# Performance work log

Measured on AMD Instinct MI355X. Metric: run time of the kernel, lower is better.

## Reference

```python
import jax, jax.numpy as jnp
import numpy as np
from jax import lax

B, CIN, H, W = 32, 256, 64, 64
K, STRIDE = 9, 2
CAPS_TYPES, OS0, OS1 = 32, 8, 1
NUM_ITER = 3
OH = (H - K) // STRIDE + 1  # 28
OW = (W - K) // STRIDE + 1  # 28
EPS = 1e-8


def squash(x):
    # Hinton squash over capsule pose dims (os0, os1)
    n2 = jnp.sum(x * x, axis=(-2, -1), keepdims=True)
    return (n2 / (1.0 + n2)) * x / jnp.sqrt(n2 + EPS)


def setup_inputs() -> dict:
    key = jax.random.key(0)
    k1, k2 = jax.random.split(key)
    x = jax.random.normal(k1, (B, CIN, H, W), jnp.float32)
    cout = CAPS_TYPES * OS0 * OS1
    conv_w = jax.random.normal(k2, (cout, CIN, K, K), jnp.float32) / np.float32(np.sqrt(CIN * K * K))
    conv_b = jnp.zeros((cout,), jnp.float32)
    routing_bias = jnp.full((CAPS_TYPES, OH, OW, OS0, OS1), 0.1, jnp.float32)
    return {"x": x, "conv_w": conv_w, "conv_b": conv_b, "routing_bias": routing_bias}


def reference(x, conv_w, conv_b, routing_bias):
    b = x.shape[0]
    caps = lax.conv_general_dilated(
        x, conv_w, (STRIDE, STRIDE), 'VALID',
        dimension_numbers=('NCHW', 'OIHW', 'NCHW'))
    caps = caps + conv_b[None, :, None, None]
    # [b, C*os0*os1, oh, ow] -> [b, C, oh, ow, os0, os1]
    caps = caps.reshape(b, CAPS_TYPES, OS0, OS1, OH, OW).transpose(0, 1, 4, 5, 2, 3)
    poses = squash(caps)
    # Dynamic routing (degenerate: one vote per output capsule, singleton input dims)
    votes = poses  # [b, C, oh, ow, os0, os1]
    logits = jnp.zeros((b, CAPS_TYPES, OH, OW), caps.dtype)
    for _ in range(NUM_ITER):
        c = jax.nn.softmax(logits, axis=1)           # couplings over output caps types
        s = c[..., None, None] * votes + routing_bias  # weighted vote sum (+ bias)
        poses = squash(s)
        logits = logits + jnp.sum(votes * poses, axis=(-2, -1))  # agreement update
    acts = jnp.sqrt(jnp.sum(poses * poses, axis=(-2, -1)))  # [b, C, oh, ow]
    return poses, acts
```

## Files before the change

### kernel.cpp

```cpp
#include <hip/hip_runtime.h>

#define B_    32
#define CIN_  256
#define H_    64
#define W_    64
#define OH_   28
#define OW_   28
#define M_TOTAL 25088
#define POSE_ELEMS 6422528

typedef _Float16 f16;
typedef _Float16 f16x8 __attribute__((ext_vector_type(8)));
typedef _Float16 f16x4 __attribute__((ext_vector_type(4)));
typedef float    f32x4 __attribute__((ext_vector_type(4)));

#define GLD_LDS16(gp, lp) __builtin_amdgcn_global_load_lds( \
    (const __attribute__((address_space(1))) void*)(gp),    \
    (__attribute__((address_space(3))) void*)(lp), 16, 0, 0)

#define SBAR()    asm volatile("s_barrier" ::: "memory")
#define WAITVM0() asm volatile("s_waitcnt vmcnt(0)" ::: "memory")
#define WAITVM4() asm volatile("s_waitcnt vmcnt(4)" ::: "memory")
#define LGKM8()   asm volatile("s_waitcnt lgkmcnt(8)" ::: "memory")

__global__ __launch_bounds__(256) void xt_kernel(const float* __restrict__ x,
                                                 f16* __restrict__ Xt)
{
    __shared__ float tile[64 * 65];
    const int t  = threadIdx.x;
    const int c0 = blockIdx.x * 64;
    const int h  = blockIdx.y;
    const int b  = blockIdx.z;

    const float* src = x + (((long)(b * CIN_ + c0)) * H_ + h) * W_;
    const int w4 = (t & 15) * 4;
    const int cr = t >> 4;
#pragma unroll
    for (int it = 0; it < 4; ++it) {
        const int c = it * 16 + cr;
        const float4 v = *(const float4*)(src + (long)c * (H_ * W_) + w4);
        tile[c * 65 + w4 + 0] = v.x;
        tile[c * 65 + w4 + 1] = v.y;
        tile[c * 65 + w4 + 2] = v.z;
        tile[c * 65 + w4 + 3] = v.w;
    }
    __syncthreads();

    f16* dst = Xt + ((long)(b * H_ + h) * W_) * CIN_ + c0;
    const int wq = t >> 4, cq = t & 15;
#pragma unroll
    for (int it = 0; it < 4; ++it) {
        const int w2 = it * 16 + wq;
        f16x4 v;
        v[0] = (f16)tile[(cq * 4 + 0) * 65 + w2];
        v[1] = (f16)tile[(cq * 4 + 1) * 65 + w2];
        v[2] = (f16)tile[(cq * 4 + 2) * 65 + w2];
        v[3] = (f16)tile[(cq * 4 + 3) * 65 + w2];
        *(f16x4*)(dst + (long)w2 * CIN_ + cq * 4) = v;
    }
}

__global__ __launch_bounds__(256) void wt_kernel(const float* __restrict__ w,
                                                 f16* __restrict__ Wt)
{
    __shared__ float tile[64 * 81];
    const int t  = threadIdx.x;
    const int co = blockIdx.x >> 2;
    const int c0 = (blockIdx.x & 3) * 64;
    const float* src = w + ((long)co * 256 + c0) * 81;
    for (int i = t; i < 64 * 81; i += 256) tile[i] = src[i];
    __syncthreads();
    for (int i = t; i < 64 * 81; i += 256) {
        const int khw = i >> 6, ci = i & 63;
        Wt[(long)khw * 65536 + co * 256 + c0 + ci] = (f16)tile[ci * 81 + khw];
    }
}

__global__ __launch_bounds__(512, 2) void gemm_kernel(const f16* __restrict__ Xt,
                                                      const f16* __restrict__ Wt,
                                                      f16* __restrict__ part,
                                                      int nsplit)
{
    __shared__ __align__(16) char lds[131072];
    char* ldsA = lds;
    char* ldsB = lds + 65536;

    const int t    = threadIdx.x;
    const int lane = t & 63, wave = t >> 6;

    const int nwg = 98 * nsplit;
    const int q = nwg >> 3, r8 = nwg & 7;
    const int xcd = blockIdx.x & 7, idx = blockIdx.x >> 3;
    const int wgid = (xcd < r8 ? xcd * (q + 1) : r8 * (q + 1) + (xcd - r8) * q) + idx;
    const int sk = wgid / 98;
    const int mt = wgid - sk * 98;
    const int m0 = mt * 256;

    const int ntb = 324 / nsplit, rem = 324 - ntb * nsplit;
    const int ksb = sk * ntb + (sk < rem ? sk : rem);
    const int NT  = ntb + (sk < rem ? 1 : 0);

    const int csrc = ((lane & 7) ^ (lane >> 3)) * 8;
    int aoff[4], boff[4];
#pragma unroll
    for (int i = 0; i < 4; ++i) {
        const int r  = (i * 8 + wave) * 8 + (lane >> 3);
        const int ga = (r & 63) + ((r >> 6) & 1) * 128 + (r >> 7) * 64;
        const int m  = m0 + ga;
        const int b   = m / 784;
        const int rem2 = m - b * 784;
        const int oh  = rem2 / 28;
        const int ow  = rem2 - oh * 28;
        aoff[i] = ((b * 64 + 2 * oh) * 64 + 2 * ow) * 256 + csrc;
        const int gb = (r & 31) + ((r >> 5) & 3) * 64 + (r >> 7) * 32;
        boff[i] = gb * 256 + csrc;
    }

    const int wm = wave >> 2, wn = wave & 3;
    int rowA[8], rowB[4];
#pragma unroll
    for (int mf = 0; mf < 8; ++mf) {
        const int g  = wm * 128 + mf * 16 + (lane & 15);
        const int lr = (g & 63) + ((g >> 6) & 1) * 128 + (g >> 7) * 64;
        rowA[mf] = lr * 128;
    }
#pragma unroll
    for (int nf = 0; nf < 4; ++nf) {
        const int g  = wn * 64 + nf * 16 + (lane & 15);
        const int lr = (g & 31) + ((g >> 6) << 5) + ((g >> 5) & 1) * 128;
        rowB[nf] = lr * 128;
    }
    int csw[2];
    csw[0] = ((lane >> 4) * 16) ^ ((lane & 7) << 4);
    csw[1] = 64 ^ csw[0];

    f32x4 acc[8][4];
    const f32x4 z = {0.f, 0.f, 0.f, 0.f};
#pragma unroll
    for (int i = 0; i < 8; ++i)
#pragma unroll
        for (int j = 0; j < 4; ++j) acc[i][j] = z;

#define KOFFS(KS, AK, BK)                                      \
    {  const int cb_ = (KS) & 3, khw_ = (KS) >> 2;             \
       const int kh_ = khw_ / 9, kw_ = khw_ - kh_ * 9;         \
       AK = (kh_ * 64 + kw_) * 256 + cb_ * 64;                 \
       BK = khw_ * 65536 + cb_ * 64; }

#define STAGE_A_HALF(H, AK, NB) do {                                               \
    GLD_LDS16(Xt + aoff[2*(H)]   + (AK), ldsA + (NB)*32768 + ((2*(H))*8   + wave)*1024); \
    GLD_LDS16(Xt + aoff[2*(H)+1] + (AK), ldsA + (NB)*32768 + ((2*(H)+1)*8 + wave)*1024); } while(0)
#define STAGE_B_HALF(H, BK, NB) do {                                               \
    GLD_LDS16(Wt + boff[2*(H)]   + (BK), ldsB + (NB)*32768 + ((2*(H))*8   + wave)*1024); \
    GLD_LDS16(Wt + boff[2*(H)+1] + (BK), ldsB + (NB)*32768 + ((2*(H)+1)*8 + wave)*1024); } while(0)

#define MFMA_PAIR(MI, NI, A, Bf)                                                        \
    acc[MI][NI] = __builtin_amdgcn_mfma_f32_16x16x32_f16((A)[0], (Bf)[0], acc[MI][NI], 0,0,0); \
    acc[MI][NI] = __builtin_amdgcn_mfma_f32_16x16x32_f16((A)[1], (Bf)[1], acc[MI][NI], 0,0,0);
#define MFMA_Q(MH, NH, BF)                                          \
    MFMA_PAIR((MH)*4+0, (NH)*2+0, af[0], BF[0]) MFMA_PAIR((MH)*4+0, (NH)*2+1, af[0], BF[1]) \
    MFMA_PAIR((MH)*4+1, (NH)*2+0, af[1], BF[0]) MFMA_PAIR((MH)*4+1, (NH)*2+1, af[1], BF[1]) \
    MFMA_PAIR((MH)*4+2, (NH)*2+0, af[2], BF[0]) MFMA_PAIR((MH)*4+2, (NH)*2+1, af[2], BF[1]) \
    MFMA_PAIR((MH)*4+3, (NH)*2+0, af[3], BF[0]) MFMA_PAIR((MH)*4+3, (NH)*2+1, af[3], BF[1])

#define READ_AF(P, MH) do {                                           \
    _Pragma("unroll")                                                 \
    for (int k_ = 0; k_ < 4; ++k_) {                                  \
        af[k_][0] = *(const f16x8*)((P) + rowA[(MH)*4+k_] + csw[0]);  \
        af[k_][1] = *(const f16x8*)((P) + rowA[(MH)*4+k_] + csw[1]);  \
    } } while(0)
#define READ_BF(P, V, NH) do {                                        \
    _Pragma("unroll")                                                 \
    for (int k_ = 0; k_ < 2; ++k_) {                                  \
        V[k_][0] = *(const f16x8*)((P) + rowB[(NH)*2+k_] + csw[0]);   \
        V[k_][1] = *(const f16x8*)((P) + rowB[(NH)*2+k_] + csw[1]);   \
    } } while(0)

    f16x8 af[4][2], bf0[2][2], bf1[2][2];

    {
        int ak0, bk0;
        KOFFS(ksb, ak0, bk0);
        STAGE_A_HALF(0, ak0, 0);
        STAGE_B_HALF(0, bk0, 0);
        STAGE_B_HALF(1, bk0, 0);
        STAGE_A_HALF(1, ak0, 0);
    }
    WAITVM4();
    SBAR();

#pragma unroll 1
    for (int tt = 0; tt < NT; ++tt) {
        const int c = tt & 1, nc = c ^ 1;
        const int ksn = ksb + ((tt + 1 < NT) ? tt + 1 : tt);
        int akn, bkn;
        KOFFS(ksn, akn, bkn);
        const char* pA = ldsA + c * 32768;
        const char* pB = ldsB + c * 32768;

        STAGE_A_HALF(0, akn, nc);
        WAITVM4();
        READ_AF(pA, 0);
        READ_BF(pB, bf0, 0);
        LGKM8();
        SBAR();
        __builtin_amdgcn_s_setprio(1);
        MFMA_Q(0, 0, bf0)
        __builtin_amdgcn_s_setprio(0);

        STAGE_B_HALF(0, bkn, nc);
        WAITVM4();
        READ_BF(pB, bf1, 1);
        SBAR();
        __builtin_amdgcn_s_setprio(1);
        MFMA_Q(0, 1, bf1)
        __builtin_amdgcn_s_setprio(0);

        STAGE_B_HALF(1, bkn, nc);
        READ_AF(pA, 1);
        SBAR();
        __builtin_amdgcn_s_setprio(1);
        MFMA_Q(1, 1, bf1)
        __builtin_amdgcn_s_setprio(0);

        STAGE_A_HALF(1, akn, nc);
        WAITVM4();
        SBAR();
        __builtin_amdgcn_s_setprio(1);
        MFMA_Q(1, 0, bf0)
        __builtin_amdgcn_s_setprio(0);
    }
    WAITVM0();

    f16* base = part + (long)sk * (M_TOTAL * 256);
    const int lrow = (lane >> 4) * 4;
#pragma unroll
    for (int nf = 0; nf < 4; ++nf) {
        const int n = wn * 64 + nf * 16 + (lane & 15);
#pragma unroll
        for (int mf = 0; mf < 8; ++mf) {
            const long mrow = m0 + wm * 128 + mf * 16 + lrow;
            f16* cw = base + mrow * 256 + n;
#pragma unroll
            for (int j = 0; j < 4; ++j) cw[(long)j * 256] = (f16)acc[mf][nf][j];
        }
    }
}

__global__ __launch_bounds__(256) void routing_kernel(const f16* __restrict__ part,
                                                      const float* __restrict__ bias,
                                                      const float* __restrict__ rb,
                                                      float* __restrict__ out, int nsplit)
{
    const int t   = threadIdx.x;
    const int m   = blockIdx.x * 8 + (t >> 5);
    const int cap = t & 31;
    const int b   = m / 784;
    const int rem = m - b * 784;
    const int oh  = rem / 28;
    const int ow  = rem - oh * 28;

    const float4 b0 = ((const float4*)(bias + cap * 8))[0];
    const float4 b1 = ((const float4*)(bias + cap * 8))[1];
    float v[8] = {b0.x, b0.y, b0.z, b0.w, b1.x, b1.y, b1.z, b1.w};
#pragma unroll 1
    for (int sk = 0; sk < nsplit; ++sk) {
        const f16x8 u = *(const f16x8*)(part + (long)sk * (M_TOTAL * 256) + (long)m * 256 + cap * 8);
#pragma unroll
        for (int j = 0; j < 8; ++j) v[j] += (float)u[j];
    }

    float n2 = 0.f;
#pragma unroll
    for (int j = 0; j < 8; ++j) n2 += v[j] * v[j];
    const float f = (n2 / (1.f + n2)) / sqrtf(n2 + 1e-8f);
    float votes[8];
#pragma unroll
    for (int j = 0; j < 8; ++j) votes[j] = f * v[j];

    const float4* rp = (const float4*)(rb + ((long)(cap * 28 + oh) * 28 + ow) * 8);
    const float4 r0 = rp[0], r1 = rp[1];
    const float rbv[8] = {r0.x, r0.y, r0.z, r0.w, r1.x, r1.y, r1.z, r1.w};

    float logit = 0.f;
    float poses[8];
#pragma unroll 1
    for (int it = 0; it < 3; ++it) {
        float mx = logit;
#pragma unroll
        for (int d = 16; d > 0; d >>= 1) mx = fmaxf(mx, __shfl_xor(mx, d, 32));
        const float e = __expf(logit - mx);
        float se = e;
#pragma unroll
        for (int d = 16; d > 0; d >>= 1) se += __shfl_xor(se, d, 32);
        const float c = e / se;

        float s[8];
        float sn2 = 0.f;
#pragma unroll
        for (int j = 0; j < 8; ++j) { s[j] = c * votes[j] + rbv[j]; sn2 += s[j] * s[j]; }
        const float sf = (sn2 / (1.f + sn2)) / sqrtf(sn2 + 1e-8f);
        float dot = 0.f;
#pragma unroll
        for (int j = 0; j < 8; ++j) { poses[j] = sf * s[j]; dot += votes[j] * poses[j]; }
        logit += dot;
    }

    float pn2 = 0.f;
#pragma unroll
    for (int j = 0; j < 8; ++j) pn2 += poses[j] * poses[j];
    const float act = sqrtf(pn2);

    float* po = out + (((long)(b * 32 + cap) * 28 + oh) * 28 + ow) * 8;
    float4 o0 = {poses[0], poses[1], poses[2], poses[3]};
    float4 o1 = {poses[4], poses[5], poses[6], poses[7]};
    ((float4*)po)[0] = o0;
    ((float4*)po)[1] = o1;
    out[POSE_ELEMS + ((long)(b * 32 + cap) * 28 + oh) * 28 + ow] = act;
}

extern "C" void kernel_launch(void* const* d_in, const int* in_sizes, int n_in,
                              void* d_out, int out_size, void* d_ws, size_t ws_size,
                              hipStream_t stream)
{
    const float* x      = (const float*)d_in[0];
    const float* conv_w = (const float*)d_in[1];
    const float* conv_b = (const float*)d_in[2];
    const float* rb     = (const float*)d_in[3];
    float* out          = (float*)d_out;

    char* ws = (char*)d_ws;
    f16*   Xt   = (f16*)ws;
    f16*   Wt   = (f16*)(ws + 67108864);
    const size_t base = 67108864 + 10616832;
    f16* part = (f16*)(ws + base);
    const size_t part_bytes = (size_t)M_TOTAL * 256 * 2;

    int nsplit = 1;
    if      (ws_size >= base + 5 * part_bytes) nsplit = 5;
    else if (ws_size >= base + 4 * part_bytes) nsplit = 4;
    else if (ws_size >= base + 2 * part_bytes) nsplit = 2;

    xt_kernel<<<dim3(4, 64, 32), 256, 0, stream>>>(x, Xt);
    wt_kernel<<<dim3(1024), 256, 0, stream>>>(conv_w, Wt);
    gemm_kernel<<<dim3(98 * nsplit), dim3(512), 0, stream>>>(Xt, Wt, part, nsplit);
    routing_kernel<<<dim3(3136), 256, 0, stream>>>(part, conv_b, rb, out, nsplit);
}
```

Before: 292.6 us.

## Load weight fragments directly from global in MFMA order, bypassing LDS

The weight-transpose kernel now writes the B matrix pre-swizzled into MFMA fragment order. The GEMM loads each wave's B fragments straight from global memory into registers instead of staging them through LDS. This halves LDS use, removes the B LDS reads, and cuts the barriers per K-step from four to two, merging the MFMA quarters into two phases. The trade-off is that B global-load latency is now only hidden by one phase of work. Waves that share the same B columns also re-fetch it through the cache.

```diff
diff --git a/kernel.cpp b/kernel.cpp
--- a/kernel.cpp
+++ b/kernel.cpp
@@ -20,8 +20,7 @@
 
 #define SBAR()    asm volatile("s_barrier" ::: "memory")
 #define WAITVM0() asm volatile("s_waitcnt vmcnt(0)" ::: "memory")
-#define WAITVM4() asm volatile("s_waitcnt vmcnt(4)" ::: "memory")
-#define LGKM8()   asm volatile("s_waitcnt lgkmcnt(8)" ::: "memory")
+#define WAITVM2() asm volatile("s_waitcnt vmcnt(2)" ::: "memory")
 
 __global__ __launch_bounds__(256) void xt_kernel(const float* __restrict__ x,
                                                  f16* __restrict__ Xt)
@@ -66,13 +65,22 @@
     __shared__ float tile[64 * 81];
     const int t  = threadIdx.x;
     const int co = blockIdx.x >> 2;
-    const int c0 = (blockIdx.x & 3) * 64;
-    const float* src = w + ((long)co * 256 + c0) * 81;
+    const int cb = blockIdx.x & 3;
+    const float* src = w + ((long)co * 256 + cb * 64) * 81;
     for (int i = t; i < 64 * 81; i += 256) tile[i] = src[i];
     __syncthreads();
-    for (int i = t; i < 64 * 81; i += 256) {
-        const int khw = i >> 6, ci = i & 63;
-        Wt[(long)khw * 65536 + co * 256 + c0 + ci] = (f16)tile[ci * 81 + khw];
+
+    const int n16 = co >> 4, llo = co & 15;
+    for (int i = t; i < 648; i += 256) {
+        const int khw = i >> 3;
+        const int rem = i & 7;
+        const int h = rem >> 2, lhi = rem & 3;
+        const int k0 = h * 32 + lhi * 8;
+        f16x8 v;
+#pragma unroll
+        for (int e = 0; e < 8; ++e) v[e] = (f16)tile[(k0 + e) * 81 + khw];
+        const long off = ((long)(khw * 4 + cb) * 2048 + n16 * 128 + h * 64 + lhi * 16 + llo) * 8;
+        *(f16x8*)(Wt + off) = v;
     }
 }
 
@@ -81,9 +89,7 @@
                                                       f16* __restrict__ part,
                                                       int nsplit)
 {
-    __shared__ __align__(16) char lds[131072];
-    char* ldsA = lds;
-    char* ldsB = lds + 65536;
+    __shared__ __align__(16) char ldsA[65536];
 
     const int t    = threadIdx.x;
     const int lane = t & 63, wave = t >> 6;
@@ -101,7 +107,7 @@
     const int NT  = ntb + (sk < rem ? 1 : 0);
 
     const int csrc = ((lane & 7) ^ (lane >> 3)) * 8;
-    int aoff[4], boff[4];
+    int aoff[4];
 #pragma unroll
     for (int i = 0; i < 4; ++i) {
         const int r  = (i * 8 + wave) * 8 + (lane >> 3);
@@ -112,27 +118,20 @@
         const int oh  = rem2 / 28;
         const int ow  = rem2 - oh * 28;
         aoff[i] = ((b * 64 + 2 * oh) * 64 + 2 * ow) * 256 + csrc;
-        const int gb = (r & 31) + ((r >> 5) & 3) * 64 + (r >> 7) * 32;
-        boff[i] = gb * 256 + csrc;
     }
 
     const int wm = wave >> 2, wn = wave & 3;
-    int rowA[8], rowB[4];
+    int rowA[8];
 #pragma unroll
     for (int mf = 0; mf < 8; ++mf) {
         const int g  = wm * 128 + mf * 16 + (lane & 15);
         const int lr = (g & 63) + ((g >> 6) & 1) * 128 + (g >> 7) * 64;
         rowA[mf] = lr * 128;
     }
-#pragma unroll
-    for (int nf = 0; nf < 4; ++nf) {
-        const int g  = wn * 64 + nf * 16 + (lane & 15);
-        const int lr = (g & 31) + ((g >> 6) << 5) + ((g >> 5) & 1) * 128;
-        rowB[nf] = lr * 128;
-    }
     int csw[2];
     csw[0] = ((lane >> 4) * 16) ^ ((lane & 7) << 4);
     csw[1] = 64 ^ csw[0];
+    const f16* Bbase = Wt + wn * 4096 + lane * 8;
 
     f32x4 acc[8][4];
     const f32x4 z = {0.f, 0.f, 0.f, 0.f};
@@ -141,18 +140,26 @@
 #pragma unroll
         for (int j = 0; j < 4; ++j) acc[i][j] = z;
 
-#define KOFFS(KS, AK, BK)                                      \
+#define KOFFS_A(KS, AK)                                        \
     {  const int cb_ = (KS) & 3, khw_ = (KS) >> 2;             \
        const int kh_ = khw_ / 9, kw_ = khw_ - kh_ * 9;         \
-       AK = (kh_ * 64 + kw_) * 256 + cb_ * 64;                 \
-       BK = khw_ * 65536 + cb_ * 64; }
+       AK = (kh_ * 64 + kw_) * 256 + cb_ * 64; }
 
 #define STAGE_A_HALF(H, AK, NB) do {                                               \
     GLD_LDS16(Xt + aoff[2*(H)]   + (AK), ldsA + (NB)*32768 + ((2*(H))*8   + wave)*1024); \
     GLD_LDS16(Xt + aoff[2*(H)+1] + (AK), ldsA + (NB)*32768 + ((2*(H)+1)*8 + wave)*1024); } while(0)
-#define STAGE_B_HALF(H, BK, NB) do {                                               \
-    GLD_LDS16(Wt + boff[2*(H)]   + (BK), ldsB + (NB)*32768 + ((2*(H))*8   + wave)*1024); \
-    GLD_LDS16(Wt + boff[2*(H)+1] + (BK), ldsB + (NB)*32768 + ((2*(H)+1)*8 + wave)*1024); } while(0)
+
+#define LOAD_B(KS) do {                                        \
+    const f16* bp_ = Bbase + (long)(KS) * 16384;               \
+    bf0[0][0] = *(const f16x8*)(bp_ + 0);                      \
+    bf0[0][1] = *(const f16x8*)(bp_ + 512);                    \
+    bf0[1][0] = *(const f16x8*)(bp_ + 1024);                   \
+    bf0[1][1] = *(const f16x8*)(bp_ + 1536);                   \
+    bf1[0][0] = *(const f16x8*)(bp_ + 2048);                   \
+    bf1[0][1] = *(const f16x8*)(bp_ + 2560);                   \
+    bf1[1][0] = *(const f16x8*)(bp_ + 3072);                   \
+    bf1[1][1] = *(const f16x8*)(bp_ + 3584);                   \
+} while(0)
 
 #define MFMA_PAIR(MI, NI, A, Bf)                                                        \
     acc[MI][NI] = __builtin_amdgcn_mfma_f32_16x16x32_f16((A)[0], (Bf)[0], acc[MI][NI], 0,0,0); \
@@ -169,66 +176,42 @@
         af[k_][0] = *(const f16x8*)((P) + rowA[(MH)*4+k_] + csw[0]);  \
         af[k_][1] = *(const f16x8*)((P) + rowA[(MH)*4+k_] + csw[1]);  \
     } } while(0)
-#define READ_BF(P, V, NH) do {                                        \
-    _Pragma("unroll")                                                 \
-    for (int k_ = 0; k_ < 2; ++k_) {                                  \
-        V[k_][0] = *(const f16x8*)((P) + rowB[(NH)*2+k_] + csw[0]);   \
-        V[k_][1] = *(const f16x8*)((P) + rowB[(NH)*2+k_] + csw[1]);   \
-    } } while(0)
 
     f16x8 af[4][2], bf0[2][2], bf1[2][2];
 
     {
-        int ak0, bk0;
-        KOFFS(ksb, ak0, bk0);
+        int ak0;
+        KOFFS_A(ksb, ak0);
         STAGE_A_HALF(0, ak0, 0);
-        STAGE_B_HALF(0, bk0, 0);
-        STAGE_B_HALF(1, bk0, 0);
         STAGE_A_HALF(1, ak0, 0);
-    }
-    WAITVM4();
-    SBAR();
+        LOAD_B(ksb);
+    }
 
 #pragma unroll 1
     for (int tt = 0; tt < NT; ++tt) {
         const int c = tt & 1, nc = c ^ 1;
         const int ksn = ksb + ((tt + 1 < NT) ? tt + 1 : tt);
-        int akn, bkn;
-        KOFFS(ksn, akn, bkn);
+        int akn;
+        KOFFS_A(ksn, akn);
         const char* pA = ldsA + c * 32768;
-        const char* pB = ldsB + c * 32768;
 
         STAGE_A_HALF(0, akn, nc);
-        WAITVM4();
+        WAITVM2();
+        SBAR();
         READ_AF(pA, 0);
-        READ_BF(pB, bf0, 0);
-        LGKM8();
-        SBAR();
         __builtin_amdgcn_s_setprio(1);
         MFMA_Q(0, 0, bf0)
-        __builtin_amdgcn_s_setprio(0);
-
-        STAGE_B_HALF(0, bkn, nc);
-        WAITVM4();
-        READ_BF(pB, bf1, 1);
-        SBAR();
-        __builtin_amdgcn_s_setprio(1);
         MFMA_Q(0, 1, bf1)
         __builtin_amdgcn_s_setprio(0);
 
-        STAGE_B_HALF(1, bkn, nc);
+        STAGE_A_HALF(1, akn, nc);
         READ_AF(pA, 1);
-        SBAR();
         __builtin_amdgcn_s_setprio(1);
+        MFMA_Q(1, 0, bf0)
         MFMA_Q(1, 1, bf1)
         __builtin_amdgcn_s_setprio(0);
-
-        STAGE_A_HALF(1, akn, nc);
-        WAITVM4();
+        LOAD_B(ksn);
         SBAR();
-        __builtin_amdgcn_s_setprio(1);
-        MFMA_Q(1, 0, bf0)
-        __builtin_amdgcn_s_setprio(0);
     }
     WAITVM0();
 
```

After: 302.3 us. 3.3% more time.
